# Optimization experiments

Hardware: AMD Instinct MI355X
Metric: run time of the kernel (lower is better)

Reference implementation:

```python
import jax, jax.numpy as jnp
import numpy as np

B, DIM, H = 64, 768, 12
WH, WW = 14, 14
N = WH * WW + 1  # 197
HD = DIM // H    # 64
NUM_REL = (2 * WH - 1) * (2 * WW - 1) + 3  # 732


def _relative_position_index(wh, ww):
    coords = np.stack(np.meshgrid(np.arange(wh), np.arange(ww), indexing='ij'))  # [2,wh,ww]
    flat = coords.reshape(2, -1)                                                # [2, wh*ww]
    rel = flat[:, :, None] - flat[:, None, :]                                   # [2, M, M]
    rel = rel.transpose(1, 2, 0).astype(np.int64)                               # [M, M, 2]
    rel[:, :, 0] += wh - 1
    rel[:, :, 1] += ww - 1
    rel[:, :, 0] *= 2 * ww - 1
    nrd = (2 * wh - 1) * (2 * ww - 1) + 3
    m = wh * ww
    idx = np.zeros((m + 1, m + 1), dtype=np.int32)
    idx[1:, 1:] = rel.sum(-1)
    idx[0, :] = nrd - 3
    idx[:, 0] = nrd - 2
    idx[0, 0] = nrd - 1
    return idx


def setup_inputs() -> dict:
    key = jax.random.key(0)
    ks = jax.random.split(key, 7)
    x = jax.random.normal(ks[0], (B, N, DIM), dtype=jnp.float32)
    Wqkv = jax.random.normal(ks[1], (3 * DIM, DIM), dtype=jnp.float32) * 0.02
    q_bias = jax.random.normal(ks[2], (DIM,), dtype=jnp.float32) * 0.02
    v_bias = jax.random.normal(ks[3], (DIM,), dtype=jnp.float32) * 0.02
    rel_table = jax.random.normal(ks[4], (NUM_REL, H), dtype=jnp.float32) * 0.02
    Wproj = jax.random.normal(ks[5], (DIM, DIM), dtype=jnp.float32) * 0.02
    bproj = jax.random.normal(ks[6], (DIM,), dtype=jnp.float32) * 0.02
    rel_index = jnp.asarray(_relative_position_index(WH, WW))  # [N, N] int32
    return {"x": x, "Wqkv": Wqkv, "q_bias": q_bias, "v_bias": v_bias,
            "rel_table": rel_table, "Wproj": Wproj, "bproj": bproj,
            "rel_index": rel_index}


def reference(x, Wqkv, q_bias, v_bias, rel_table, Wproj, bproj, rel_index):
    b, n, c = x.shape
    hd = Wqkv.shape[0] // (3 * H)
    scale = hd ** -0.5
    qkv_bias = jnp.concatenate([q_bias, jnp.zeros_like(v_bias), v_bias])
    qkv = x @ Wqkv.T + qkv_bias                              # [B,N,3*DIM]
    qkv = qkv.reshape(b, n, 3, H, hd).transpose(2, 0, 3, 1, 4)  # [3,B,H,N,hd]
    q, k, v = qkv[0] * scale, qkv[1], qkv[2]
    attn = jnp.einsum('bhqd,bhkd->bhqk', q, k)               # [B,H,N,N]
    rel_bias = rel_table[rel_index].transpose(2, 0, 1)       # [H,N,N]
    attn = jax.nn.softmax(attn + rel_bias[None], axis=-1)
    out = jnp.einsum('bhqk,bhkd->bhqd', attn, v)             # [B,H,N,hd]
    out = out.transpose(0, 2, 1, 3).reshape(b, n, -1)        # [B,N,DIM]
    return out @ Wproj.T + bproj
```

## Files before the change

### kernel.cpp

```cpp
#include <hip/hip_runtime.h>

typedef _Float16 f16_t;
typedef f16_t f16x8 __attribute__((ext_vector_type(8)));
typedef float f32x4 __attribute__((ext_vector_type(4)));

#define DEVI __device__ __forceinline__

constexpr int NB    = 64;
constexpr int NTOK  = 197;
constexpr int NH    = 12;
constexpr int DIM   = 768;
constexpr int M_TOK = NB * NTOK;
constexpr int NPAD  = 224;
constexpr float SCALE = 0.125f;

constexpr int KP_SZ  = 2 * NPAD * 32;
constexpr int VTS_SZ = 7 * 64 * 32;
constexpr int P_LD   = 228;
constexpr int PW_SZ  = 16 * P_LD;
constexpr int ATTN_LDS = (KP_SZ + VTS_SZ + 8 * PW_SZ) * 2;

DEVI ushort f2h_bits(float f) { _Float16 h = (_Float16)f; return __builtin_bit_cast(ushort, h); }

DEVI void gload16(const void* g, void* l) {
    __builtin_amdgcn_global_load_lds((const __attribute__((address_space(1))) void*)g,
                                     (__attribute__((address_space(3))) void*)l, 16, 0, 0);
}

DEVI int xcd_swz(int orig, int nwg) {
    const int q = nwg >> 3, r = nwg & 7;
    const int xcd = orig & 7, idx = orig >> 3;
    return (xcd < r ? xcd * (q + 1) : r * (q + 1) + (xcd - r) * q) + idx;
}

__global__ __launch_bounds__(256) void k_pre(const float* __restrict__ s0, ushort* __restrict__ d0, int n0,
                                             const float* __restrict__ s1, ushort* __restrict__ d1, int n1,
                                             const float* __restrict__ s2, ushort* __restrict__ d2, int n2,
                                             int ncvtblk,
                                             const float* __restrict__ rel_table,
                                             const int* __restrict__ rel_index,
                                             ushort* __restrict__ biash) {
    if ((int)blockIdx.x < ncvtblk) {
        int i = blockIdx.x * 256 + threadIdx.x;
        const float* s; ushort* d;
        if (i < n0)           { s = s0; d = d0; }
        else if (i < n0 + n1) { i -= n0; s = s1; d = d1; }
        else                  { i -= n0 + n1; if (i >= n2) return; s = s2; d = d2; }
        float4 v = reinterpret_cast<const float4*>(s)[i];
        ushort4 o;
        o.x = f2h_bits(v.x); o.y = f2h_bits(v.y); o.z = f2h_bits(v.z); o.w = f2h_bits(v.w);
        reinterpret_cast<ushort4*>(d)[i] = o;
    } else {
        int idx = (blockIdx.x - ncvtblk) * 256 + threadIdx.x;
        if (idx >= NH * NPAD * 256) return;
        const int j  = idx & 15;
        const int fr = (idx >> 4) & 15;
        const int i  = (idx >> 8) % NPAD;
        const int h  = (idx >> 8) / NPAD;
        const int col = j * 16 + fr;
        float v = -30000.f;
        if (i < NTOK && col < NTOK && j < 14) v = rel_table[rel_index[i * NTOK + col] * NH + h];
        biash[idx] = f2h_bits(v);
    }
}

__global__ __launch_bounds__(512, 2) void k_qkv8(const ushort* __restrict__ A, const ushort* __restrict__ BT,
                                                 const float* __restrict__ b_q, const float* __restrict__ b_v,
                                                 ushort* __restrict__ outp) {
    constexpr int M = M_TOK, N = 2304, K = 768, nt = K / 64;
    constexpr int NWG = (N / 256) * 50;
    extern __shared__ ushort lds[];
    ushort* ldsA = lds;
    ushort* ldsB = lds + 32768;
    const int tid = threadIdx.x, wid = tid >> 6, lane = tid & 63;
    const int wm = wid >> 2, wn = wid & 3;
    const int fr = lane & 15, fg = lane >> 4;
    const int bid = xcd_swz(blockIdx.y * (N / 256) + blockIdx.x, NWG);
    const int m0 = (bid / (N / 256)) * 256, n0 = (bid % (N / 256)) * 256;

    const int srow = tid >> 2;
    const int sc = ((tid & 3) ^ ((tid >> 3) & 3)) * 8;
    int ra0 = m0 + srow;       ra0 = ra0 < M ? ra0 : M - 1;
    int ra1 = m0 + srow + 128; ra1 = ra1 < M ? ra1 : M - 1;
    const ushort* pA0 = A + (size_t)ra0 * K + sc;
    const ushort* pA1 = A + (size_t)ra1 * K + sc;
    const ushort* pB0 = BT + (size_t)(n0 + srow) * K + sc;
    const ushort* pB1 = BT + (size_t)(n0 + srow + 128) * K + sc;
    const int dstt = tid * 8;

    int aoff[8], boff[4];
#pragma unroll
    for (int mi = 0; mi < 8; ++mi) {
        const int r = wm * 128 + mi * 16 + fr;
        aoff[mi] = r * 32 + ((fg ^ ((r >> 1) & 3)) * 8);
    }
#pragma unroll
    for (int j = 0; j < 4; ++j) {
        const int c = wn * 64 + j * 16 + fr;
        boff[j] = c * 32 + ((fg ^ ((c >> 1) & 3)) * 8);
    }

    f32x4 acc[8][4] = {};
    f16x8 av[8];

    auto STAGE = [&](int T, int isA, int k) {
        const int Tw = T >= nt ? T - nt : T;
        const size_t so = (size_t)(Tw * 64 + k * 32);
        const int db = (T & 1) * 16384 + k * 8192 + dstt;
        if (isA) { gload16(pA0 + so, ldsA + db); gload16(pA1 + so, ldsA + db + 4096); }
        else     { gload16(pB0 + so, ldsB + db); gload16(pB1 + so, ldsB + db + 4096); }
    };

#define LDA8(B_, KS_) { _Pragma("unroll") for (int mi = 0; mi < 8; ++mi) \
        av[mi] = *(const f16x8*)(ldsA + (B_) * 16384 + (KS_) * 8192 + aoff[mi]); }

#define PHASE(B_, KS_, NH_, LA_, ST_T, ST_A, ST_K, GATE_) { \
        if (LA_) LDA8(B_, KS_); \
        f16x8 bv0 = *(const f16x8*)(ldsB + (B_) * 16384 + (KS_) * 8192 + boff[(NH_) * 2]); \
        f16x8 bv1 = *(const f16x8*)(ldsB + (B_) * 16384 + (KS_) * 8192 + boff[(NH_) * 2 + 1]); \
        STAGE(ST_T, ST_A, ST_K); \
        __builtin_amdgcn_s_barrier(); \
        __builtin_amdgcn_s_setprio(1); \
        _Pragma("unroll") for (int mi = 0; mi < 8; ++mi) { \
            acc[mi][(NH_) * 2]     = __builtin_amdgcn_mfma_f32_16x16x32_f16(av[mi], bv0, acc[mi][(NH_) * 2], 0, 0, 0); \
            acc[mi][(NH_) * 2 + 1] = __builtin_amdgcn_mfma_f32_16x16x32_f16(av[mi], bv1, acc[mi][(NH_) * 2 + 1], 0, 0, 0); } \
        __builtin_amdgcn_s_setprio(0); \
        asm volatile("s_waitcnt lgkmcnt(0)" ::: "memory"); \
        __builtin_amdgcn_sched_barrier(0); \
        if (GATE_) { asm volatile("s_waitcnt vmcnt(4)" ::: "memory"); __builtin_amdgcn_sched_barrier(0); } \
        __builtin_amdgcn_s_barrier(); }

    STAGE(0, 1, 0); STAGE(0, 0, 0); STAGE(0, 1, 1); STAGE(0, 0, 1);
    STAGE(1, 1, 0); STAGE(1, 0, 0);
    asm volatile("s_waitcnt vmcnt(4)" ::: "memory");
    __builtin_amdgcn_sched_barrier(0);
    __builtin_amdgcn_s_barrier();

    for (int i = 0; i < nt / 2; ++i) {
        const int t0 = 2 * i;
        PHASE(0, 0, 0, 1, t0 + 1, 1, 1, 0)
        PHASE(0, 0, 1, 0, t0 + 1, 0, 1, 0)
        PHASE(0, 1, 0, 1, t0 + 2, 1, 0, 0)
        PHASE(0, 1, 1, 0, t0 + 2, 0, 0, 1)
        PHASE(1, 0, 0, 1, t0 + 2, 1, 1, 0)
        PHASE(1, 0, 1, 0, t0 + 2, 0, 1, 0)
        PHASE(1, 1, 0, 1, t0 + 3, 1, 0, 0)
        PHASE(1, 1, 1, 0, t0 + 3, 0, 0, 1)
    }
#undef PHASE
#undef LDA8

    asm volatile("s_waitcnt vmcnt(0) lgkmcnt(0)" ::: "memory");
    __builtin_amdgcn_sched_barrier(0);
    __builtin_amdgcn_s_barrier();

    ushort* ws = lds + wid * 8192;
#pragma unroll
    for (int ni = 0; ni < 4; ++ni) {
        const int col = n0 + wn * 64 + ni * 16 + fr;
        float addv, mul;
        if (col < 768)       { addv = b_q[col]; mul = SCALE; }
        else if (col < 1536) { addv = 0.f; mul = 1.f; }
        else                 { addv = b_v[col - 1536]; mul = 1.f; }
#pragma unroll
        for (int mi = 0; mi < 8; ++mi)
#pragma unroll
            for (int r = 0; r < 4; ++r)
                ws[(mi * 16 + fg * 4 + r) * 64 + ni * 16 + fr] = f2h_bits((acc[mi][ni][r] + addv) * mul);
    }
    __syncthreads();
#pragma unroll
    for (int it = 0; it < 16; ++it) {
        const int g = it * 64 + lane;
        const int r = g >> 3, seg = g & 7;
        const int row = m0 + wm * 128 + r;
        uint4 v = *(const uint4*)(ws + r * 64 + seg * 8);
        if (row < M) *(uint4*)(outp + (size_t)row * N + n0 + wn * 64 + seg * 8) = v;
    }
}

__global__ __launch_bounds__(256) void k_proj(const ushort* __restrict__ A, const ushort* __restrict__ BT,
                                              int M, int N, int K, int nwg,
                                              const float* __restrict__ b_p,
                                              float* __restrict__ out_f) {
    __shared__ __align__(16) ushort lds[2][8192];
    const int tid = threadIdx.x, wid = tid >> 6, lane = tid & 63;
    const int wm = wid >> 1, wn = wid & 1;
    const int fr = lane & 15, fg = lane >> 4;
    const int nbx = N / 128;
    const int bid = xcd_swz(blockIdx.y * nbx + blockIdx.x, nwg);
    const int m0 = (bid / nbx) * 128, n0 = (bid % nbx) * 128;

    int rA[2], rB[2], cs[2], dst[2];
#pragma unroll
    for (int i = 0; i < 2; ++i) {
        const int g = (wid * 2 + i) * 64 + lane;
        const int row = g >> 2, sp = g & 3;
        cs[i]  = (sp ^ ((row >> 1) & 3)) * 8;
        dst[i] = (wid * 2 + i) * 512;
        const int ra = m0 + row;
        rA[i] = ra < M ? ra : M - 1;
        rB[i] = n0 + row;
    }

    f32x4 acc[4][4] = {};
    const int nt = K / 32;

    auto stage = [&](int t, int buf) {
#pragma unroll
        for (int i = 0; i < 2; ++i)
            gload16(A + (size_t)rA[i] * K + t * 32 + cs[i], &lds[buf][dst[i]]);
#pragma unroll
        for (int i = 0; i < 2; ++i)
            gload16(BT + (size_t)rB[i] * K + t * 32 + cs[i], &lds[buf][4096 + dst[i]]);
    };

    stage(0, 0);
    __syncthreads();
    for (int t = 0; t < nt; ++t) {
        const int cur = t & 1;
        if (t + 1 < nt) stage(t + 1, cur ^ 1);
        const ushort* As = lds[cur];
        const ushort* Bs = lds[cur] + 4096;
        f16x8 af[4], bf[4];
#pragma unroll
        for (int i = 0; i < 4; ++i) {
            const int r = wm * 64 + i * 16 + fr;
            af[i] = *(const f16x8*)(As + r * 32 + ((fg ^ ((r >> 1) & 3)) * 8));
        }
#pragma unroll
        for (int i = 0; i < 4; ++i) {
            const int c = wn * 64 + i * 16 + fr;
            bf[i] = *(const f16x8*)(Bs + c * 32 + ((fg ^ ((c >> 1) & 3)) * 8));
        }
#pragma unroll
        for (int mi = 0; mi < 4; ++mi)
#pragma unroll
            for (int ni = 0; ni < 4; ++ni)
                acc[mi][ni] = __builtin_amdgcn_mfma_f32_16x16x32_f16(af[mi], bf[ni], acc[mi][ni], 0, 0, 0);
        __syncthreads();
    }

    float* wsf = reinterpret_cast<float*>(&lds[0][0]) + wid * 2048;
#pragma unroll
    for (int half = 0; half < 2; ++half) {
#pragma unroll
        for (int ni = 0; ni < 4; ++ni) {
            const int col = n0 + wn * 64 + ni * 16 + fr;
            const float addv = b_p[col];
#pragma unroll
            for (int mi2 = 0; mi2 < 2; ++mi2) {
                const int mi = half * 2 + mi2;
#pragma unroll
                for (int r = 0; r < 4; ++r) {
                    const int lrow = mi2 * 16 + fg * 4 + r;
                    wsf[lrow * 64 + ((ni * 16 + fr) ^ (((lrow >> 2) & 3) << 4))] = acc[mi][ni][r] + addv;
                }
            }
        }
#pragma unroll
        for (int it = 0; it < 8; ++it) {
            const int g = it * 64 + lane;
            const int lrow = g >> 4, seg = g & 15;
            const int srcc = (seg * 4) ^ (((lrow >> 2) & 3) << 4);
            float4 v = *reinterpret_cast<const float4*>(wsf + lrow * 64 + srcc);
            const int row = m0 + wm * 64 + half * 32 + lrow;
            if (row < M)
                *reinterpret_cast<float4*>(out_f + (size_t)row * N + n0 + wn * 64 + seg * 4) = v;
        }
    }
}

__global__ __launch_bounds__(512) void k_attn(const ushort* __restrict__ qkv,
                                              const ushort* __restrict__ biash, ushort* __restrict__ out) {
    extern __shared__ ushort sm[];
    ushort* kp  = sm;
    ushort* vts = sm + KP_SZ;
    ushort* ps  = sm + KP_SZ + VTS_SZ;
    const int tid = threadIdx.x, wid = tid >> 6, lane = tid & 63;
    const int fr = lane & 15, fg = lane >> 4;
    const int bh = blockIdx.x;
    const int b = bh / NH, h = bh % NH;
    const size_t qb = (size_t)(b * NTOK) * 2304;
    const int swz8 = (fg ^ ((fr >> 1) & 3)) * 8;

    ushort* vtile = ps;
    for (int t = tid; t < NPAD * 8; t += 512) {
        const int row = t >> 3, seg = t & 7;
        uint4 kv = make_uint4(0u, 0u, 0u, 0u), vv = make_uint4(0u, 0u, 0u, 0u);
        if (row < NTOK) {
            const ushort* src = qkv + qb + (size_t)row * 2304 + 768 + h * 64;
            kv = *reinterpret_cast<const uint4*>(src + seg * 8);
            vv = *reinterpret_cast<const uint4*>(src + 768 + seg * 8);
        }
        const int pcg = (seg & 3) ^ ((row >> 1) & 3);
        *reinterpret_cast<uint4*>(kp + (seg >> 2) * (NPAD * 32) + row * 32 + pcg * 8) = kv;
        *reinterpret_cast<uint4*>(vtile + row * 72 + seg * 8) = vv;
    }
    __syncthreads();
    for (int o = tid; o < 7 * 64 * 4; o += 512) {
        const int kc = o >> 8, rem = o & 255, d = rem >> 2, pcg = rem & 3;
        const int k0 = kc * 32 + (pcg ^ ((d >> 1) & 3)) * 8;
        ushort w[8];
#pragma unroll
        for (int e = 0; e < 8; ++e) w[e] = vtile[(k0 + e) * 72 + d];
        uint4 val;
        val.x = (uint)w[0] | ((uint)w[1] << 16);
        val.y = (uint)w[2] | ((uint)w[3] << 16);
        val.z = (uint)w[4] | ((uint)w[5] << 16);
        val.w = (uint)w[6] | ((uint)w[7] << 16);
        *reinterpret_cast<uint4*>(vts + kc * 2048 + d * 32 + pcg * 8) = val;
    }
    __syncthreads();

    ushort* pw = ps + wid * PW_SZ;

    for (int s = wid; s < 13; s += 8) {
        const int q0 = s * 16;
        f16x8 qf[2];
        {
            int row = q0 + fr;
            row = row < NTOK ? row : NTOK - 1;
            const ushort* qp = qkv + qb + (size_t)row * 2304 + h * 64 + fg * 8;
            qf[0] = *reinterpret_cast<const f16x8*>(qp);
            qf[1] = *reinterpret_cast<const f16x8*>(qp + 32);
        }
        f32x4 sacc[14] = {};
#pragma unroll
        for (int j = 0; j < 14; ++j) {
#pragma unroll
            for (int kh = 0; kh < 2; ++kh) {
                f16x8 kf = *reinterpret_cast<const f16x8*>(kp + kh * (NPAD * 32) + (j * 16 + fr) * 32 + swz8);
                sacc[j] = __builtin_amdgcn_mfma_f32_16x16x32_f16(qf[kh], kf, sacc[j], 0, 0, 0);
            }
        }
        float rs4[4];
#pragma unroll
        for (int r = 0; r < 4; ++r) {
            const int qrow_l = fg * 4 + r;
            int qrow = q0 + qrow_l;
            qrow = qrow < NTOK ? qrow : NTOK - 1;
            const ushort* bp16 = biash + (((size_t)(h * NPAD + qrow) * 16 + fr) << 4);
            f16x8 bv0 = *reinterpret_cast<const f16x8*>(bp16);
            f16x8 bv1 = *reinterpret_cast<const f16x8*>(bp16 + 8);
            float mx = -1e30f;
#pragma unroll
            for (int j = 0; j < 14; ++j) {
                const float bj = (float)(j < 8 ? bv0[j] : bv1[j - 8]);
                float v = sacc[j][r] + bj;
                sacc[j][r] = v;
                mx = fmaxf(mx, v);
            }
            mx = fmaxf(mx, __shfl_xor(mx, 1));
            mx = fmaxf(mx, __shfl_xor(mx, 2));
            mx = fmaxf(mx, __shfl_xor(mx, 4));
            mx = fmaxf(mx, __shfl_xor(mx, 8));
            float sum = 0.f;
            ushort* prow = pw + qrow_l * P_LD;
#pragma unroll
            for (int j = 0; j < 14; ++j) {
                float p = __expf(sacc[j][r] - mx);
                sum += p;
                prow[j * 16 + fr] = f2h_bits(p);
            }
            sum += __shfl_xor(sum, 1);
            sum += __shfl_xor(sum, 2);
            sum += __shfl_xor(sum, 4);
            sum += __shfl_xor(sum, 8);
            rs4[r] = sum;
        }
        f32x4 o[4] = {};
#pragma unroll
        for (int kc = 0; kc < 7; ++kc) {
            f16x8 af = *reinterpret_cast<const f16x8*>(pw + fr * P_LD + kc * 32 + fg * 8);
#pragma unroll
            for (int dt = 0; dt < 4; ++dt) {
                f16x8 bv = *reinterpret_cast<const f16x8*>(vts + kc * 2048 + (dt * 16 + fr) * 32 + swz8);
                o[dt] = __builtin_amdgcn_mfma_f32_16x16x32_f16(af, bv, o[dt], 0, 0, 0);
            }
        }
#pragma unroll
        for (int dt = 0; dt < 4; ++dt) {
#pragma unroll
            for (int r = 0; r < 4; ++r) {
                const int qrow = q0 + fg * 4 + r;
                if (qrow < NTOK) {
                    const float val = o[dt][r] / rs4[r];
                    out[(size_t)(b * NTOK + qrow) * DIM + h * 64 + dt * 16 + fr] = f2h_bits(val);
                }
            }
        }
    }
}

extern "C" void kernel_launch(void* const* d_in, const int* in_sizes, int n_in,
                              void* d_out, int out_size, void* d_ws, size_t ws_size,
                              hipStream_t stream) {
    const float* x         = (const float*)d_in[0];
    const float* Wqkv      = (const float*)d_in[1];
    const float* q_bias    = (const float*)d_in[2];
    const float* v_bias    = (const float*)d_in[3];
    const float* rel_table = (const float*)d_in[4];
    const float* Wproj     = (const float*)d_in[5];
    const float* bproj     = (const float*)d_in[6];
    const int*   rel_index = (const int*)d_in[7];
    float* out = (float*)d_out;

    char* p = (char*)d_ws;
    auto alloc = [&](size_t bytes) { char* r = p; p += (bytes + 255) & ~(size_t)255; return r; };
    ushort* xb     = (ushort*)alloc((size_t)M_TOK * DIM * 2);
    ushort* wqkvb  = (ushort*)alloc((size_t)2304 * 768 * 2);
    ushort* wprojb = (ushort*)alloc((size_t)768 * 768 * 2);
    ushort* qkvb   = (ushort*)alloc((size_t)M_TOK * 2304 * 2);
    ushort* biasb  = (ushort*)alloc((size_t)NH * NPAD * 256 * 2);
    ushort* aob    = (ushort*)alloc((size_t)M_TOK * DIM * 2);

    (void)hipFuncSetAttribute((const void*)k_qkv8, hipFuncAttributeMaxDynamicSharedMemorySize, 131072);
    (void)hipFuncSetAttribute((const void*)k_attn, hipFuncAttributeMaxDynamicSharedMemorySize, ATTN_LDS);

    const int n0 = M_TOK * DIM / 4, n1 = 2304 * 768 / 4, n2 = 768 * 768 / 4;
    const int ncvtblk = (n0 + n1 + n2 + 255) / 256;
    const int nbiasblk = (NH * NPAD * 256 + 255) / 256;
    k_pre<<<ncvtblk + nbiasblk, 256, 0, stream>>>(x, xb, n0, Wqkv, wqkvb, n1, Wproj, wprojb, n2,
                                                  ncvtblk, rel_table, rel_index, biasb);

    k_qkv8<<<dim3(2304 / 256, (M_TOK + 255) / 256), 512, 131072, stream>>>(
        xb, wqkvb, q_bias, v_bias, qkvb);
    k_attn<<<dim3(NB * NH), 512, ATTN_LDS, stream>>>(qkvb, biasb, aob);
    k_proj<<<dim3(768 / 128, (M_TOK + 127) / 128), 256, 0, stream>>>(
        aob, wprojb, M_TOK, 768, 768, (768 / 128) * ((M_TOK + 127) / 128),
        bproj, out);
}
```

Measured before the change: 147.1 us.

## Compute transposed scores in attention to keep probabilities in registers

The QK^T MFMA now takes K as the A operand and Q as the B operand, so each lane holds a column of scores for one query row. This lets softmax reduce with two cross-lane shuffles and feed the probabilities straight into the PV MFMA as packed f16 registers, with no trip through LDS. The V transpose is done directly during the global load, which removes the staging tile, one barrier and the LDS P buffer, shrinking LDS per block. The bias layout is reshaped to match the new fragment ordering, and output stores become vectorized ushort4 writes.

```diff
diff --git a/kernel.cpp b/kernel.cpp
--- a/kernel.cpp
+++ b/kernel.cpp
@@ -16,9 +16,7 @@
 
 constexpr int KP_SZ  = 2 * NPAD * 32;
 constexpr int VTS_SZ = 7 * 64 * 32;
-constexpr int P_LD   = 228;
-constexpr int PW_SZ  = 16 * P_LD;
-constexpr int ATTN_LDS = (KP_SZ + VTS_SZ + 8 * PW_SZ) * 2;
+constexpr int ATTN_LDS = (KP_SZ + VTS_SZ) * 2;
 
 DEVI ushort f2h_bits(float f) { _Float16 h = (_Float16)f; return __builtin_bit_cast(ushort, h); }
 
@@ -52,14 +50,17 @@
         reinterpret_cast<ushort4*>(d)[i] = o;
     } else {
         int idx = (blockIdx.x - ncvtblk) * 256 + threadIdx.x;
-        if (idx >= NH * NPAD * 256) return;
-        const int j  = idx & 15;
-        const int fr = (idx >> 4) & 15;
-        const int i  = (idx >> 8) % NPAD;
-        const int h  = (idx >> 8) / NPAD;
-        const int col = j * 16 + fr;
+        if (idx >= NH * NPAD * 224) return;
+        const int r    = idx & 3;
+        const int rest = idx >> 2;
+        const int j    = rest % 14;
+        const int rest2 = rest / 14;
+        const int fg   = rest2 & 3;
+        const int q    = (rest2 >> 2) % NPAD;
+        const int h    = (rest2 >> 2) / NPAD;
+        const int kt   = j * 16 + fg * 4 + r;
         float v = -30000.f;
-        if (i < NTOK && col < NTOK && j < 14) v = rel_table[rel_index[i * NTOK + col] * NH + h];
+        if (q < NTOK && kt < NTOK) v = rel_table[rel_index[q * NTOK + kt] * NH + h];
         biash[idx] = f2h_bits(v);
     }
 }
@@ -276,7 +277,6 @@
     extern __shared__ ushort sm[];
     ushort* kp  = sm;
     ushort* vts = sm + KP_SZ;
-    ushort* ps  = sm + KP_SZ + VTS_SZ;
     const int tid = threadIdx.x, wid = tid >> 6, lane = tid & 63;
     const int fr = lane & 15, fg = lane >> 4;
     const int bh = blockIdx.x;
@@ -284,7 +284,6 @@
     const size_t qb = (size_t)(b * NTOK) * 2304;
     const int swz8 = (fg ^ ((fr >> 1) & 3)) * 8;
 
-    ushort* vtile = ps;
     for (int t = tid; t < NPAD * 8; t += 512) {
         const int row = t >> 3, seg = t & 7;
         uint4 kv = make_uint4(0u, 0u, 0u, 0u), vv = make_uint4(0u, 0u, 0u, 0u);
@@ -295,99 +294,88 @@
         }
         const int pcg = (seg & 3) ^ ((row >> 1) & 3);
         *reinterpret_cast<uint4*>(kp + (seg >> 2) * (NPAD * 32) + row * 32 + pcg * 8) = kv;
-        *reinterpret_cast<uint4*>(vtile + row * 72 + seg * 8) = vv;
+        const int m = row >> 5, tt = row & 31;
+        const int s = ((tt >> 2) & 3) * 8 + ((tt >> 4) << 2) + (tt & 3);
+        const ushort* vw = reinterpret_cast<const ushort*>(&vv);
+#pragma unroll
+        for (int e = 0; e < 8; ++e) {
+            const int d = seg * 8 + e;
+            const int pg = (s >> 3) ^ ((d >> 1) & 3);
+            vts[m * 2048 + d * 32 + pg * 8 + (s & 7)] = vw[e];
+        }
     }
     __syncthreads();
-    for (int o = tid; o < 7 * 64 * 4; o += 512) {
-        const int kc = o >> 8, rem = o & 255, d = rem >> 2, pcg = rem & 3;
-        const int k0 = kc * 32 + (pcg ^ ((d >> 1) & 3)) * 8;
-        ushort w[8];
-#pragma unroll
-        for (int e = 0; e < 8; ++e) w[e] = vtile[(k0 + e) * 72 + d];
-        uint4 val;
-        val.x = (uint)w[0] | ((uint)w[1] << 16);
-        val.y = (uint)w[2] | ((uint)w[3] << 16);
-        val.z = (uint)w[4] | ((uint)w[5] << 16);
-        val.w = (uint)w[6] | ((uint)w[7] << 16);
-        *reinterpret_cast<uint4*>(vts + kc * 2048 + d * 32 + pcg * 8) = val;
-    }
-    __syncthreads();
-
-    ushort* pw = ps + wid * PW_SZ;
-
-    for (int s = wid; s < 13; s += 8) {
-        const int q0 = s * 16;
-        f16x8 qf[2];
-        {
-            int row = q0 + fr;
-            row = row < NTOK ? row : NTOK - 1;
-            const ushort* qp = qkv + qb + (size_t)row * 2304 + h * 64 + fg * 8;
-            qf[0] = *reinterpret_cast<const f16x8*>(qp);
-            qf[1] = *reinterpret_cast<const f16x8*>(qp + 32);
-        }
+
+    for (int st = wid; st < 13; st += 8) {
+        const int q0 = st * 16;
+        int qrow = q0 + fr;
+        qrow = qrow < NTOK ? qrow : NTOK - 1;
+        const ushort* qp = qkv + qb + (size_t)qrow * 2304 + h * 64 + fg * 8;
+        const f16x8 qf0 = *reinterpret_cast<const f16x8*>(qp);
+        const f16x8 qf1 = *reinterpret_cast<const f16x8*>(qp + 32);
+        const ushort* bp = biash + ((size_t)(h * NPAD + qrow) * 4 + fg) * 56;
+        f16x8 bias[7];
+#pragma unroll
+        for (int i = 0; i < 7; ++i) bias[i] = *reinterpret_cast<const f16x8*>(bp + i * 8);
+
         f32x4 sacc[14] = {};
 #pragma unroll
         for (int j = 0; j < 14; ++j) {
-#pragma unroll
-            for (int kh = 0; kh < 2; ++kh) {
-                f16x8 kf = *reinterpret_cast<const f16x8*>(kp + kh * (NPAD * 32) + (j * 16 + fr) * 32 + swz8);
-                sacc[j] = __builtin_amdgcn_mfma_f32_16x16x32_f16(qf[kh], kf, sacc[j], 0, 0, 0);
-            }
-        }
-        float rs4[4];
-#pragma unroll
-        for (int r = 0; r < 4; ++r) {
-            const int qrow_l = fg * 4 + r;
-            int qrow = q0 + qrow_l;
-            qrow = qrow < NTOK ? qrow : NTOK - 1;
-            const ushort* bp16 = biash + (((size_t)(h * NPAD + qrow) * 16 + fr) << 4);
-            f16x8 bv0 = *reinterpret_cast<const f16x8*>(bp16);
-            f16x8 bv1 = *reinterpret_cast<const f16x8*>(bp16 + 8);
-            float mx = -1e30f;
-#pragma unroll
-            for (int j = 0; j < 14; ++j) {
-                const float bj = (float)(j < 8 ? bv0[j] : bv1[j - 8]);
-                float v = sacc[j][r] + bj;
+            const f16x8 kf0 = *reinterpret_cast<const f16x8*>(kp + (j * 16 + fr) * 32 + swz8);
+            const f16x8 kf1 = *reinterpret_cast<const f16x8*>(kp + NPAD * 32 + (j * 16 + fr) * 32 + swz8);
+            sacc[j] = __builtin_amdgcn_mfma_f32_16x16x32_f16(kf0, qf0, sacc[j], 0, 0, 0);
+            sacc[j] = __builtin_amdgcn_mfma_f32_16x16x32_f16(kf1, qf1, sacc[j], 0, 0, 0);
+        }
+        float mx = -1e30f;
+#pragma unroll
+        for (int j = 0; j < 14; ++j)
+#pragma unroll
+            for (int r = 0; r < 4; ++r) {
+                const int bi = j * 4 + r;
+                const float v = sacc[j][r] + (float)bias[bi >> 3][bi & 7];
                 sacc[j][r] = v;
                 mx = fmaxf(mx, v);
             }
-            mx = fmaxf(mx, __shfl_xor(mx, 1));
-            mx = fmaxf(mx, __shfl_xor(mx, 2));
-            mx = fmaxf(mx, __shfl_xor(mx, 4));
-            mx = fmaxf(mx, __shfl_xor(mx, 8));
-            float sum = 0.f;
-            ushort* prow = pw + qrow_l * P_LD;
-#pragma unroll
-            for (int j = 0; j < 14; ++j) {
-                float p = __expf(sacc[j][r] - mx);
+        mx = fmaxf(mx, __shfl_xor(mx, 16));
+        mx = fmaxf(mx, __shfl_xor(mx, 32));
+        float sum = 0.f;
+#pragma unroll
+        for (int j = 0; j < 14; ++j)
+#pragma unroll
+            for (int r = 0; r < 4; ++r) {
+                const float p = __expf(sacc[j][r] - mx);
+                sacc[j][r] = p;
                 sum += p;
-                prow[j * 16 + fr] = f2h_bits(p);
             }
-            sum += __shfl_xor(sum, 1);
-            sum += __shfl_xor(sum, 2);
-            sum += __shfl_xor(sum, 4);
-            sum += __shfl_xor(sum, 8);
-            rs4[r] = sum;
-        }
+        sum += __shfl_xor(sum, 16);
+        sum += __shfl_xor(sum, 32);
+
         f32x4 o[4] = {};
 #pragma unroll
-        for (int kc = 0; kc < 7; ++kc) {
-            f16x8 af = *reinterpret_cast<const f16x8*>(pw + fr * P_LD + kc * 32 + fg * 8);
+        for (int m = 0; m < 7; ++m) {
+            uint4 pk;
+            pk.x = __builtin_bit_cast(uint, __builtin_amdgcn_cvt_pkrtz(sacc[2 * m][0], sacc[2 * m][1]));
+            pk.y = __builtin_bit_cast(uint, __builtin_amdgcn_cvt_pkrtz(sacc[2 * m][2], sacc[2 * m][3]));
+            pk.z = __builtin_bit_cast(uint, __builtin_amdgcn_cvt_pkrtz(sacc[2 * m + 1][0], sacc[2 * m + 1][1]));
+            pk.w = __builtin_bit_cast(uint, __builtin_amdgcn_cvt_pkrtz(sacc[2 * m + 1][2], sacc[2 * m + 1][3]));
+            const f16x8 pa = __builtin_bit_cast(f16x8, pk);
 #pragma unroll
             for (int dt = 0; dt < 4; ++dt) {
-                f16x8 bv = *reinterpret_cast<const f16x8*>(vts + kc * 2048 + (dt * 16 + fr) * 32 + swz8);
-                o[dt] = __builtin_amdgcn_mfma_f32_16x16x32_f16(af, bv, o[dt], 0, 0, 0);
+                const f16x8 av = *reinterpret_cast<const f16x8*>(vts + m * 2048 + (dt * 16 + fr) * 32 + swz8);
+                o[dt] = __builtin_amdgcn_mfma_f32_16x16x32_f16(av, pa, o[dt], 0, 0, 0);
             }
         }
-#pragma unroll
-        for (int dt = 0; dt < 4; ++dt) {
-#pragma unroll
-            for (int r = 0; r < 4; ++r) {
-                const int qrow = q0 + fg * 4 + r;
-                if (qrow < NTOK) {
-                    const float val = o[dt][r] / rs4[r];
-                    out[(size_t)(b * NTOK + qrow) * DIM + h * 64 + dt * 16 + fr] = f2h_bits(val);
-                }
+        const float inv = 1.f / sum;
+        if (q0 + fr < NTOK) {
+            ushort* op = out + (size_t)(b * NTOK + q0 + fr) * DIM + h * 64 + fg * 4;
+#pragma unroll
+            for (int dt = 0; dt < 4; ++dt) {
+                ushort4 w;
+                w.x = f2h_bits(o[dt][0] * inv);
+                w.y = f2h_bits(o[dt][1] * inv);
+                w.z = f2h_bits(o[dt][2] * inv);
+                w.w = f2h_bits(o[dt][3] * inv);
+                *reinterpret_cast<ushort4*>(op + dt * 16) = w;
             }
         }
     }
@@ -412,7 +400,7 @@
     ushort* wqkvb  = (ushort*)alloc((size_t)2304 * 768 * 2);
     ushort* wprojb = (ushort*)alloc((size_t)768 * 768 * 2);
     ushort* qkvb   = (ushort*)alloc((size_t)M_TOK * 2304 * 2);
-    ushort* biasb  = (ushort*)alloc((size_t)NH * NPAD * 256 * 2);
+    ushort* biasb  = (ushort*)alloc((size_t)NH * NPAD * 224 * 2);
     ushort* aob    = (ushort*)alloc((size_t)M_TOK * DIM * 2);
 
     (void)hipFuncSetAttribute((const void*)k_qkv8, hipFuncAttributeMaxDynamicSharedMemorySize, 131072);
@@ -420,7 +408,7 @@
 
     const int n0 = M_TOK * DIM / 4, n1 = 2304 * 768 / 4, n2 = 768 * 768 / 4;
     const int ncvtblk = (n0 + n1 + n2 + 255) / 256;
-    const int nbiasblk = (NH * NPAD * 256 + 255) / 256;
+    const int nbiasblk = (NH * NPAD * 224 + 255) / 256;
     k_pre<<<ncvtblk + nbiasblk, 256, 0, stream>>>(x, xb, n0, Wqkv, wqkvb, n1, Wproj, wprojb, n2,
                                                   ncvtblk, rel_table, rel_index, biasb);
 
```

Result: slower. 177.4 us (+20.6%).
